# Kernel tuning notes

Measured on AMD Instinct MI355X. Metric: run time of the kernel, lower is better.

## Reference

```python
import jax, jax.numpy as jnp
import numpy as np

K = 3  # kernel_size
STRIDE, PAD, DIL = 1, 1, 1


def conv2d(x, w, b):
    out = jax.lax.conv_general_dilated(
        x, w, (STRIDE, STRIDE), [(PAD, PAD), (PAD, PAD)],
        rhs_dilation=(DIL, DIL), dimension_numbers=('NCHW', 'OIHW', 'NCHW'))
    return out + b[None, :, None, None]


def bilinear_sample(x, sy, sx):
    """grid_sample(mode=bilinear, padding_mode=zeros, align_corners=True).
    x: (B,C,H,W); sy,sx: (B,K2,Ho,Wo) pixel coords. Returns (B,C,K2,Ho,Wo)."""
    B, C, H, W = x.shape
    y0 = jnp.floor(sy); x0 = jnp.floor(sx)
    y1 = y0 + 1.0;      x1 = x0 + 1.0
    wy1 = sy - y0; wy0 = 1.0 - wy1
    wx1 = sx - x0; wx0 = 1.0 - wx1
    x_flat = x.reshape(B, C, H * W)

    def gather(iy, ix):
        mask = ((iy >= 0) & (iy <= H - 1) & (ix >= 0) & (ix <= W - 1)).astype(x.dtype)
        iyc = jnp.clip(iy, 0, H - 1).astype(jnp.int32)
        ixc = jnp.clip(ix, 0, W - 1).astype(jnp.int32)
        idx = (iyc * W + ixc).reshape(B, 1, -1)
        v = jnp.take_along_axis(x_flat, idx, axis=2).reshape(B, C, *iy.shape[1:])
        return v * mask[:, None]

    return (gather(y0, x0) * (wy0 * wx0)[:, None]
            + gather(y0, x1) * (wy0 * wx1)[:, None]
            + gather(y1, x0) * (wy1 * wx0)[:, None]
            + gather(y1, x1) * (wy1 * wx1)[:, None])


def setup_inputs() -> dict:
    key = jax.random.key(0)
    ks = jax.random.split(key, 6)
    B, C, H, W = 4, 64, 128, 128
    O = 64
    x = jax.random.normal(ks[0], (B, C, H, W), jnp.float32)
    weight = jax.random.normal(ks[1], (O, C, K, K), jnp.float32) * (1.0 / (C * K * K) ** 0.5)
    bias = jax.random.normal(ks[2], (O,), jnp.float32) * 0.1
    offset_w = jax.random.normal(ks[3], (2 * K * K, C, K, K), jnp.float32) * 0.1 / (C * K * K) ** 0.5
    offset_b = jnp.zeros((2 * K * K,), jnp.float32)
    mod_w = jax.random.normal(ks[4], (K * K, C, K, K), jnp.float32) * (1.0 / (C * K * K) ** 0.5)
    mod_b = jnp.ones((K * K,), jnp.float32)
    return {"x": x, "weight": weight, "bias": bias,
            "offset_w": offset_w, "offset_b": offset_b,
            "mod_w": mod_w, "mod_b": mod_b}


def reference(x, weight, bias, offset_w, offset_b, mod_w, mod_b):
    B, C, H, W = x.shape
    O = weight.shape[0]
    K2 = K * K
    Ho = (H + 2 * PAD - DIL * (K - 1) - 1) // STRIDE + 1
    Wo = (W + 2 * PAD - DIL * (K - 1) - 1) // STRIDE + 1

    offsets = conv2d(x, offset_w, offset_b)                # (B, 2*K2, Ho, Wo)
    modul = jax.nn.sigmoid(conv2d(x, mod_w, mod_b))        # (B, K2, Ho, Wo)

    off = offsets.reshape(B, 2, K2, Ho, Wo)
    off_y, off_x = off[:, 0], off[:, 1]

    base_y, base_x = jnp.meshgrid(jnp.arange(Ho, dtype=jnp.float32),
                                  jnp.arange(Wo, dtype=jnp.float32), indexing='ij')
    base_y = base_y * STRIDE - PAD + (K // 2) * DIL
    base_x = base_x * STRIDE - PAD + (K // 2) * DIL
    koffs = jnp.arange(-(K // 2), K // 2 + 1, dtype=jnp.float32)
    ky, kx = jnp.meshgrid(koffs, koffs, indexing='ij')
    ky = ky.reshape(-1); kx = kx.reshape(-1)               # (K2,)

    sample_y = base_y[None, None] + ky[None, :, None, None] + off_y  # (B,K2,Ho,Wo)
    sample_x = base_x[None, None] + kx[None, :, None, None] + off_x
    # torch code normalizes to [-1,1] with align_corners=True; pixel coords are
    # recovered identically, so we sample directly at (sample_y, sample_x).

    sampled = bilinear_sample(x, sample_y, sample_x)       # (B,C,K2,Ho,Wo)

    w_flat = weight.reshape(O, C, K2)
    out = jnp.einsum('bckhw,ock->bohw', sampled, w_flat)   # groups=1

    mod_mean = jnp.mean(modul, axis=1, keepdims=True)      # (B,1,Ho,Wo)
    out = out * mod_mean + bias[None, :, None, None]
    return out
```

## Files before the change

### kernel.cpp

```cpp
#include <hip/hip_runtime.h>
#include <math.h>

#define K 3
#define K2 9
#define BB 4
#define C 64
#define H 128
#define W 128
#define O 64
#define HW (H*W)
#define Ho 128
#define Wo 128
#define TILE 64
#define CG 16
#define NCHUNK 4
#define KCH 144
#define NSTEP 5
#define SA_STRIDE 164

typedef _Float16 half4v __attribute__((ext_vector_type(4)));
typedef _Float16 half8v __attribute__((ext_vector_type(8)));
typedef float float4v __attribute__((ext_vector_type(4)));

__device__ __forceinline__ half8v load_frag_lds(const _Float16* p) {
    half4v a = *(const half4v*)p;
    half4v b = *(const half4v*)(p + 4);
    return __builtin_shufflevector(a, b, 0, 1, 2, 3, 4, 5, 6, 7);
}
__device__ __forceinline__ void store16_lds(_Float16* d, half8v v) {
    *(half4v*)d       = __builtin_shufflevector(v, v, 0, 1, 2, 3);
    *(half4v*)(d + 4) = __builtin_shufflevector(v, v, 4, 5, 6, 7);
}

__global__ __launch_bounds__(256) void make_xh(const float* __restrict__ x,
                                               _Float16* __restrict__ xh)
{
    __shared__ _Float16 tile[W][68];
    int by = blockIdx.x;
    int y = by % H, b = by / H;
    int t = threadIdx.x;
    int xp = t & 127, ch0 = t >> 7;
    for (int g = 0; g < 32; g++) {
        int c = g * 2 + ch0;
        tile[xp][c] = (_Float16)x[(((size_t)b * C + c) * H + y) * W + xp];
    }
    __syncthreads();
    int xp2 = t >> 1, hf = t & 1;
    const _Float16* src = &tile[xp2][hf * 32];
    _Float16* dst = xh + (((size_t)b * H + y) * W + xp2) * 64 + hf * 32;
    #pragma unroll
    for (int i = 0; i < 8; i++)
        *(half4v*)(dst + i * 4) = *(const half4v*)(src + i * 4);
}

__global__ void prep_weights(const float* __restrict__ weight,
                             const float* __restrict__ offset_w,
                             const float* __restrict__ mod_w,
                             _Float16* __restrict__ wB,
                             _Float16* __restrict__ wAB)
{
    int i = blockIdx.x * blockDim.x + threadIdx.x;
    if (i < NCHUNK * NSTEP * 4 * 64 * 8) {
        int jj = i & 7;
        int lane = (i >> 3) & 63;
        int q = (i >> 9) & 3;
        int i2 = i >> 11;
        int cc = i2 / NSTEP, s = i2 % NSTEP;
        int k = s * 32 + ((lane >> 4) & 3) * 8 + jj;
        int o = q * 16 + (lane & 15);
        float wv = 0.f;
        if (k < KCH) {
            int tap = k >> 4, cl = k & 15;
            int c = cc * CG + cl;
            wv = weight[(o * C + c) * 9 + tap];
        }
        wB[i] = (_Float16)wv;
    }
    if (i < NCHUNK * NSTEP * 2 * 64 * 8) {
        int jj = i & 7;
        int lane = (i >> 3) & 63;
        int jt = (i >> 9) & 1;
        int i2 = i >> 10;
        int cc = i2 / NSTEP, s = i2 % NSTEP;
        int k = s * 32 + ((lane >> 4) & 3) * 8 + jj;
        int n = jt * 16 + (lane & 15);
        float wv = 0.f;
        if (k < KCH && n < 27) {
            int tap = k >> 4, cl = k & 15;
            int c = cc * CG + cl;
            wv = (n < 18) ? offset_w[(n * C + c) * 9 + tap]
                          : mod_w[((n - 18) * C + c) * 9 + tap];
        }
        wAB[i] = (_Float16)wv;
    }
}

__global__ __launch_bounds__(256) void fused_kernel(
    const _Float16* __restrict__ xh,
    const _Float16* __restrict__ wB,
    const _Float16* __restrict__ wAB,
    const float* __restrict__ bias,
    const float* __restrict__ offset_b,
    const float* __restrict__ mod_b,
    float* __restrict__ out)
{
    __shared__ _Float16 s_A[TILE][SA_STRIDE];
    __shared__ unsigned int s_ai[K2 * TILE];
    __shared__ float4v s_wgt[K2 * TILE];
    __shared__ float s_res[27 * 65];
    __shared__ float s_mm[TILE];
    float* s_out = (float*)&s_A[0][0];

    int blk = blockIdx.x;
    int xcd = blk & 7, idx = blk >> 3;
    int b  = xcd >> 1;
    int h  = ((xcd & 1) << 6) | (idx >> 1);
    int wt = idx & 1;
    int t  = threadIdx.x;
    int px = t & 63;
    int q  = t >> 6;
    int lane = t & 63;
    int m16 = lane & 15;
    int quad = (lane >> 4) & 3;
    int w0 = wt * TILE;
    int wp = w0 + px;

    for (int z = t; z < TILE * 16; z += 256)
        s_A[z >> 4][KCH + (z & 15)] = (_Float16)0.f;

    const _Float16* xb = xh + (size_t)b * HW * 64;

    float4v acc2[2];
    #pragma unroll
    for (int jt = 0; jt < 2; jt++) { float4v z = {0.f,0.f,0.f,0.f}; acc2[jt] = z; }

    #pragma unroll 1
    for (int cc = 0; cc < NCHUNK; cc++) {
        __syncthreads();
        #pragma unroll
        for (int ti = 0; ti < 3; ti++) {
            if (ti == 2 && q != 0) break;
            int tap = (ti < 2) ? (2 * q + ti) : 8;
            int ki = tap / 3, kj = tap % 3;
            int y = h + ki - 1;
            int xv = wp + kj - 1;
            float m = ((y >= 0 && y < H) ? 1.f : 0.f) * ((xv >= 0 && xv < W) ? 1.f : 0.f);
            int yc = min(max(y, 0), H - 1), xcl = min(max(xv, 0), W - 1);
            const _Float16* src = xb + ((size_t)yc * W + xcl) * 64 + cc * CG;
            half8v v0 = *(const half8v*)src;
            half8v v1 = *(const half8v*)(src + 8);
            _Float16 mh = (_Float16)m;
            half8v vm = {mh, mh, mh, mh, mh, mh, mh, mh};
            v0 *= vm; v1 *= vm;
            _Float16* d = &s_A[px][tap * 16];
            store16_lds(d, v0);
            store16_lds(d + 8, v1);
        }
        __syncthreads();

        int row = q * 16 + m16;
        #pragma unroll
        for (int s = 0; s < NSTEP; s++) {
            int koff = s * 32 + quad * 8;
            half8v af = load_frag_lds(&s_A[row][koff]);
            #pragma unroll
            for (int jt = 0; jt < 2; jt++) {
                int widx = (((cc * NSTEP + s) * 2 + jt) * 64 + lane) * 8;
                half8v bf = *(const half8v*)(wAB + widx);
                acc2[jt] = __builtin_amdgcn_mfma_f32_16x16x32_f16(af, bf, acc2[jt], 0, 0, 0);
            }
        }
    }
    __syncthreads();
    #pragma unroll
    for (int jt = 0; jt < 2; jt++) {
        int n = jt * 16 + m16;
        if (n < 27) {
            #pragma unroll
            for (int r = 0; r < 4; r++)
                s_res[n * 65 + q * 16 + quad * 4 + r] = acc2[jt][r];
        }
    }
    __syncthreads();

    #pragma unroll
    for (int ee = 0; ee < 3; ee++) {
        int e = t + ee * 256;
        if (e < K2 * TILE) {
            int k = e >> 6, p = e & 63;
            float offy = s_res[k * 65 + p] + offset_b[k];
            float offx = s_res[(9 + k) * 65 + p] + offset_b[9 + k];
            float sy = (float)(h + k / 3 - 1) + offy;
            float sx = (float)(w0 + p + k % 3 - 1) + offx;
            float fy = floorf(sy), fx = floorf(sx);
            int y0 = (int)fy, x0 = (int)fx;
            float wy1 = sy - fy, wx1 = sx - fx;
            int y0c = min(max(y0, 0), H - 1), y1c = min(max(y0 + 1, 0), H - 1);
            int x0c = min(max(x0, 0), W - 1), x1c = min(max(x0 + 1, 0), W - 1);
            s_ai[e] = (unsigned int)(y0c * W + x0c)
                    | ((unsigned int)(x1c - x0c) << 14)
                    | ((unsigned int)(y1c - y0c) << 15);
            float4v wg;
            wg[0] = (1.f - wy1) * ((y0 >= 0 && y0 < H) ? 1.f : 0.f);
            wg[1] = wy1 * ((y0 + 1 >= 0 && y0 + 1 < H) ? 1.f : 0.f);
            wg[2] = (1.f - wx1) * ((x0 >= 0 && x0 < W) ? 1.f : 0.f);
            wg[3] = wx1 * ((x0 + 1 >= 0 && x0 + 1 < W) ? 1.f : 0.f);
            s_wgt[e] = wg;
        }
    }
    if (t < TILE) {
        float sm = 0.f;
        #pragma unroll
        for (int m = 0; m < 9; m++) {
            float z = s_res[(18 + m) * 65 + t] + mod_b[m];
            sm += 1.f / (1.f + expf(-z));
        }
        s_mm[t] = sm * (1.f / 9.f);
    }

    float4v acc[4];
    #pragma unroll
    for (int i = 0; i < 4; i++) { float4v z = {0.f,0.f,0.f,0.f}; acc[i] = z; }

    #pragma unroll 1
    for (int cc = 0; cc < NCHUNK; cc++) {
        __syncthreads();
        #pragma unroll
        for (int ti = 0; ti < 3; ti++) {
            if (ti == 2 && q != 0) break;
            int tap = (ti < 2) ? (2 * q + ti) : 8;
            int e = tap * 64 + px;
            unsigned int ai = s_ai[e];
            float4v wg = s_wgt[e];
            float w00f = wg[0] * wg[2], w01f = wg[0] * wg[3];
            float w10f = wg[1] * wg[2], w11f = wg[1] * wg[3];
            int a00 = ai & 0x3FFF;
            int dxo = ((ai >> 14) & 1) * 64;
            int dyo = ((ai >> 15) & 1) * (W * 64);
            const _Float16* base = xb + (size_t)a00 * 64 + cc * CG;
            half8v r00a = *(const half8v*)(base);
            half8v r00b = *(const half8v*)(base + 8);
            half8v r01a = *(const half8v*)(base + dxo);
            half8v r01b = *(const half8v*)(base + dxo + 8);
            half8v r10a = *(const half8v*)(base + dyo);
            half8v r10b = *(const half8v*)(base + dyo + 8);
            half8v r11a = *(const half8v*)(base + dyo + dxo);
            half8v r11b = *(const half8v*)(base + dyo + dxo + 8);
            _Float16 w00 = (_Float16)w00f, w01 = (_Float16)w01f;
            _Float16 w10 = (_Float16)w10f, w11 = (_Float16)w11f;
            half8v vw00 = {w00,w00,w00,w00,w00,w00,w00,w00};
            half8v vw01 = {w01,w01,w01,w01,w01,w01,w01,w01};
            half8v vw10 = {w10,w10,w10,w10,w10,w10,w10,w10};
            half8v vw11 = {w11,w11,w11,w11,w11,w11,w11,w11};
            half8v va = r00a * vw00 + r01a * vw01 + r10a * vw10 + r11a * vw11;
            half8v vb = r00b * vw00 + r01b * vw01 + r10b * vw10 + r11b * vw11;
            _Float16* d = &s_A[px][tap * 16];
            store16_lds(d, va);
            store16_lds(d + 8, vb);
        }
        __syncthreads();

        #pragma unroll
        for (int s = 0; s < NSTEP; s++) {
            int widx = (((cc * NSTEP + s) * 4 + q) * 64 + lane) * 8;
            half8v bf = *(const half8v*)(wB + widx);
            int koff = s * 32 + quad * 8;
            #pragma unroll
            for (int i = 0; i < 4; i++) {
                half8v af = load_frag_lds(&s_A[i * 16 + m16][koff]);
                acc[i] = __builtin_amdgcn_mfma_f32_16x16x32_f16(af, bf, acc[i], 0, 0, 0);
            }
        }
    }

    __syncthreads();
    #pragma unroll
    for (int i = 0; i < 4; i++) {
        int o = q * 16 + m16;
        #pragma unroll
        for (int r = 0; r < 4; r++)
            s_out[o * 65 + i * 16 + quad * 4 + r] = acc[i][r];
    }
    __syncthreads();
    {
        float mm = s_mm[px];
        #pragma unroll
        for (int jj = 0; jj < 16; jj++) {
            int o = q * 16 + jj;
            out[(((size_t)b * O + o) * Ho + h) * Wo + w0 + px] =
                s_out[o * 65 + px] * mm + bias[o];
        }
    }
}

extern "C" void kernel_launch(void* const* d_in, const int* in_sizes, int n_in,
                              void* d_out, int out_size, void* d_ws, size_t ws_size,
                              hipStream_t stream) {
    const float* x        = (const float*)d_in[0];
    const float* weight   = (const float*)d_in[1];
    const float* bias     = (const float*)d_in[2];
    const float* offset_w = (const float*)d_in[3];
    const float* offset_b = (const float*)d_in[4];
    const float* mod_w    = (const float*)d_in[5];
    const float* mod_b    = (const float*)d_in[6];
    float* out = (float*)d_out;

    _Float16* wB  = (_Float16*)d_ws;
    _Float16* wAB = wB + 40960;
    _Float16* xh  = wAB + 20480;

    prep_weights<<<160, 256, 0, stream>>>(weight, offset_w, mod_w, wB, wAB);
    make_xh<<<BB * H, 256, 0, stream>>>(x, xh);

    int nblk = BB * Ho * (Wo / TILE);
    fused_kernel<<<nblk, 256, 0, stream>>>(
        xh, wB, wAB, bias, offset_b, mod_b, out);
}
```

Measured before the change: 134.8 us.

## Merge prep kernels, vectorize x loads, alias LDS, hoist per-tap address math

Combines the weight-repack and x-transpose kernels into one launch and switches the transpose to float4 global reads. In the fused kernel, s_res is aliased onto s_A to cut LDS use, and the bilinear weights are stored as precomputed fp16 products instead of fp32 factors. Per-tap source pointers, masks and gather offsets are now computed once outside the channel-chunk loops. The goals are less launch overhead, higher occupancy and less repeated integer work. The cost is more live registers and an extra barrier, plus re-zeroing the s_A pad columns because they now share memory with s_res.

Measured after the change: 148.2 us. 9.9% more time.

```diff
diff --git a/kernel.cpp b/kernel.cpp
--- a/kernel.cpp
+++ b/kernel.cpp
@@ -31,67 +31,77 @@
     *(half4v*)d       = __builtin_shufflevector(v, v, 0, 1, 2, 3);
     *(half4v*)(d + 4) = __builtin_shufflevector(v, v, 4, 5, 6, 7);
 }
-
-__global__ __launch_bounds__(256) void make_xh(const float* __restrict__ x,
-                                               _Float16* __restrict__ xh)
+__device__ __forceinline__ half8v bcast8(_Float16 w) {
+    half8v v = {w, w, w, w, w, w, w, w};
+    return v;
+}
+
+__global__ __launch_bounds__(256) void prep_all(
+    const float* __restrict__ x,
+    const float* __restrict__ weight,
+    const float* __restrict__ offset_w,
+    const float* __restrict__ mod_w,
+    _Float16* __restrict__ xh,
+    _Float16* __restrict__ wB,
+    _Float16* __restrict__ wAB)
 {
-    __shared__ _Float16 tile[W][68];
-    int by = blockIdx.x;
-    int y = by % H, b = by / H;
     int t = threadIdx.x;
-    int xp = t & 127, ch0 = t >> 7;
-    for (int g = 0; g < 32; g++) {
-        int c = g * 2 + ch0;
-        tile[xp][c] = (_Float16)x[(((size_t)b * C + c) * H + y) * W + xp];
-    }
-    __syncthreads();
-    int xp2 = t >> 1, hf = t & 1;
-    const _Float16* src = &tile[xp2][hf * 32];
-    _Float16* dst = xh + (((size_t)b * H + y) * W + xp2) * 64 + hf * 32;
-    #pragma unroll
-    for (int i = 0; i < 8; i++)
-        *(half4v*)(dst + i * 4) = *(const half4v*)(src + i * 4);
-}
-
-__global__ void prep_weights(const float* __restrict__ weight,
-                             const float* __restrict__ offset_w,
-                             const float* __restrict__ mod_w,
-                             _Float16* __restrict__ wB,
-                             _Float16* __restrict__ wAB)
-{
-    int i = blockIdx.x * blockDim.x + threadIdx.x;
-    if (i < NCHUNK * NSTEP * 4 * 64 * 8) {
-        int jj = i & 7;
-        int lane = (i >> 3) & 63;
-        int q = (i >> 9) & 3;
-        int i2 = i >> 11;
-        int cc = i2 / NSTEP, s = i2 % NSTEP;
-        int k = s * 32 + ((lane >> 4) & 3) * 8 + jj;
-        int o = q * 16 + (lane & 15);
-        float wv = 0.f;
-        if (k < KCH) {
-            int tap = k >> 4, cl = k & 15;
-            int c = cc * CG + cl;
-            wv = weight[(o * C + c) * 9 + tap];
-        }
-        wB[i] = (_Float16)wv;
-    }
-    if (i < NCHUNK * NSTEP * 2 * 64 * 8) {
-        int jj = i & 7;
-        int lane = (i >> 3) & 63;
-        int jt = (i >> 9) & 1;
-        int i2 = i >> 10;
-        int cc = i2 / NSTEP, s = i2 % NSTEP;
-        int k = s * 32 + ((lane >> 4) & 3) * 8 + jj;
-        int n = jt * 16 + (lane & 15);
-        float wv = 0.f;
-        if (k < KCH && n < 27) {
-            int tap = k >> 4, cl = k & 15;
-            int c = cc * CG + cl;
-            wv = (n < 18) ? offset_w[(n * C + c) * 9 + tap]
-                          : mod_w[((n - 18) * C + c) * 9 + tap];
-        }
-        wAB[i] = (_Float16)wv;
+    if (blockIdx.x < BB * H) {
+        __shared__ _Float16 tile[W][68];
+        int by = blockIdx.x;
+        int y = by % H, b = by / H;
+        int xq = t & 31, cr = t >> 5;
+        #pragma unroll
+        for (int g = 0; g < 8; g++) {
+            int c = g * 8 + cr;
+            float4v v = *(const float4v*)&x[(((size_t)b * C + c) * H + y) * W + xq * 4];
+            tile[xq * 4 + 0][c] = (_Float16)v[0];
+            tile[xq * 4 + 1][c] = (_Float16)v[1];
+            tile[xq * 4 + 2][c] = (_Float16)v[2];
+            tile[xq * 4 + 3][c] = (_Float16)v[3];
+        }
+        __syncthreads();
+        int xp2 = t >> 1, hf = t & 1;
+        const _Float16* src = &tile[xp2][hf * 32];
+        _Float16* dst = xh + (((size_t)b * H + y) * W + xp2) * 64 + hf * 32;
+        #pragma unroll
+        for (int i = 0; i < 8; i++)
+            *(half4v*)(dst + i * 4) = *(const half4v*)(src + i * 4);
+    } else {
+        int i = (blockIdx.x - BB * H) * 256 + t;
+        if (i < NCHUNK * NSTEP * 4 * 64 * 8) {
+            int jj = i & 7;
+            int lane = (i >> 3) & 63;
+            int q = (i >> 9) & 3;
+            int i2 = i >> 11;
+            int cc = i2 / NSTEP, s = i2 % NSTEP;
+            int k = s * 32 + ((lane >> 4) & 3) * 8 + jj;
+            int o = q * 16 + (lane & 15);
+            float wv = 0.f;
+            if (k < KCH) {
+                int tap = k >> 4, cl = k & 15;
+                int c = cc * CG + cl;
+                wv = weight[(o * C + c) * 9 + tap];
+            }
+            wB[i] = (_Float16)wv;
+        }
+        if (i < NCHUNK * NSTEP * 2 * 64 * 8) {
+            int jj = i & 7;
+            int lane = (i >> 3) & 63;
+            int jt = (i >> 9) & 1;
+            int i2 = i >> 10;
+            int cc = i2 / NSTEP, s = i2 % NSTEP;
+            int k = s * 32 + ((lane >> 4) & 3) * 8 + jj;
+            int n = jt * 16 + (lane & 15);
+            float wv = 0.f;
+            if (k < KCH && n < 27) {
+                int tap = k >> 4, cl = k & 15;
+                int c = cc * CG + cl;
+                wv = (n < 18) ? offset_w[(n * C + c) * 9 + tap]
+                              : mod_w[((n - 18) * C + c) * 9 + tap];
+            }
+            wAB[i] = (_Float16)wv;
+        }
     }
 }
 
@@ -106,9 +116,9 @@
 {
     __shared__ _Float16 s_A[TILE][SA_STRIDE];
     __shared__ unsigned int s_ai[K2 * TILE];
-    __shared__ float4v s_wgt[K2 * TILE];
-    __shared__ float s_res[27 * 65];
+    __shared__ half4v s_wgt[K2 * TILE];
     __shared__ float s_mm[TILE];
+    float* s_res = (float*)&s_A[0][0];
     float* s_out = (float*)&s_A[0][0];
 
     int blk = blockIdx.x;
@@ -130,6 +140,20 @@
 
     const _Float16* xb = xh + (size_t)b * HW * 64;
 
+    const _Float16* srcA[3];
+    _Float16 mhA[3];
+    #pragma unroll
+    for (int ti = 0; ti < 3; ti++) {
+        int tap = (ti < 2) ? (2 * q + ti) : 8;
+        int ki = tap / 3, kj = tap % 3;
+        int y = h + ki - 1;
+        int xv = wp + kj - 1;
+        float m = ((y >= 0 && y < H) ? 1.f : 0.f) * ((xv >= 0 && xv < W) ? 1.f : 0.f);
+        int yc = min(max(y, 0), H - 1), xcl = min(max(xv, 0), W - 1);
+        srcA[ti] = xb + ((size_t)yc * W + xcl) * 64;
+        mhA[ti] = (_Float16)m;
+    }
+
     float4v acc2[2];
     #pragma unroll
     for (int jt = 0; jt < 2; jt++) { float4v z = {0.f,0.f,0.f,0.f}; acc2[jt] = z; }
@@ -141,16 +165,10 @@
         for (int ti = 0; ti < 3; ti++) {
             if (ti == 2 && q != 0) break;
             int tap = (ti < 2) ? (2 * q + ti) : 8;
-            int ki = tap / 3, kj = tap % 3;
-            int y = h + ki - 1;
-            int xv = wp + kj - 1;
-            float m = ((y >= 0 && y < H) ? 1.f : 0.f) * ((xv >= 0 && xv < W) ? 1.f : 0.f);
-            int yc = min(max(y, 0), H - 1), xcl = min(max(xv, 0), W - 1);
-            const _Float16* src = xb + ((size_t)yc * W + xcl) * 64 + cc * CG;
+            const _Float16* src = srcA[ti] + cc * CG;
             half8v v0 = *(const half8v*)src;
             half8v v1 = *(const half8v*)(src + 8);
-            _Float16 mh = (_Float16)m;
-            half8v vm = {mh, mh, mh, mh, mh, mh, mh, mh};
+            half8v vm = bcast8(mhA[ti]);
             v0 *= vm; v1 *= vm;
             _Float16* d = &s_A[px][tap * 16];
             store16_lds(d, v0);
@@ -200,12 +218,16 @@
             s_ai[e] = (unsigned int)(y0c * W + x0c)
                     | ((unsigned int)(x1c - x0c) << 14)
                     | ((unsigned int)(y1c - y0c) << 15);
-            float4v wg;
-            wg[0] = (1.f - wy1) * ((y0 >= 0 && y0 < H) ? 1.f : 0.f);
-            wg[1] = wy1 * ((y0 + 1 >= 0 && y0 + 1 < H) ? 1.f : 0.f);
-            wg[2] = (1.f - wx1) * ((x0 >= 0 && x0 < W) ? 1.f : 0.f);
-            wg[3] = wx1 * ((x0 + 1 >= 0 && x0 + 1 < W) ? 1.f : 0.f);
-            s_wgt[e] = wg;
+            float wg0 = (1.f - wy1) * ((y0 >= 0 && y0 < H) ? 1.f : 0.f);
+            float wg1 = wy1 * ((y0 + 1 >= 0 && y0 + 1 < H) ? 1.f : 0.f);
+            float wg2 = (1.f - wx1) * ((x0 >= 0 && x0 < W) ? 1.f : 0.f);
+            float wg3 = wx1 * ((x0 + 1 >= 0 && x0 + 1 < W) ? 1.f : 0.f);
+            half4v wp4;
+            wp4[0] = (_Float16)(wg0 * wg2);
+            wp4[1] = (_Float16)(wg0 * wg3);
+            wp4[2] = (_Float16)(wg1 * wg2);
+            wp4[3] = (_Float16)(wg1 * wg3);
+            s_wgt[e] = wp4;
         }
     }
     if (t < TILE) {
@@ -217,6 +239,25 @@
         }
         s_mm[t] = sm * (1.f / 9.f);
     }
+    __syncthreads();
+
+    for (int z = t; z < TILE * 16; z += 256)
+        s_A[z >> 4][KCH + (z & 15)] = (_Float16)0.f;
+
+    const _Float16* baseC[3];
+    int dxoC[3], dyoC[3];
+    half4v wgC[3];
+    #pragma unroll
+    for (int ti = 0; ti < 3; ti++) {
+        int tap = (ti < 2) ? (2 * q + ti) : 8;
+        int e = tap * 64 + px;
+        unsigned int ai = s_ai[e];
+        wgC[ti] = s_wgt[e];
+        int a00 = ai & 0x3FFF;
+        dxoC[ti] = ((ai >> 14) & 1) * 64;
+        dyoC[ti] = ((ai >> 15) & 1) * (W * 64);
+        baseC[ti] = xb + (size_t)a00 * 64;
+    }
 
     float4v acc[4];
     #pragma unroll
@@ -229,15 +270,9 @@
         for (int ti = 0; ti < 3; ti++) {
             if (ti == 2 && q != 0) break;
             int tap = (ti < 2) ? (2 * q + ti) : 8;
-            int e = tap * 64 + px;
-            unsigned int ai = s_ai[e];
-            float4v wg = s_wgt[e];
-            float w00f = wg[0] * wg[2], w01f = wg[0] * wg[3];
-            float w10f = wg[1] * wg[2], w11f = wg[1] * wg[3];
-            int a00 = ai & 0x3FFF;
-            int dxo = ((ai >> 14) & 1) * 64;
-            int dyo = ((ai >> 15) & 1) * (W * 64);
-            const _Float16* base = xb + (size_t)a00 * 64 + cc * CG;
+            const _Float16* base = baseC[ti] + cc * CG;
+            int dxo = dxoC[ti], dyo = dyoC[ti];
+            half4v wg4 = wgC[ti];
             half8v r00a = *(const half8v*)(base);
             half8v r00b = *(const half8v*)(base + 8);
             half8v r01a = *(const half8v*)(base + dxo);
@@ -246,12 +281,8 @@
             half8v r10b = *(const half8v*)(base + dyo + 8);
             half8v r11a = *(const half8v*)(base + dyo + dxo);
             half8v r11b = *(const half8v*)(base + dyo + dxo + 8);
-            _Float16 w00 = (_Float16)w00f, w01 = (_Float16)w01f;
-            _Float16 w10 = (_Float16)w10f, w11 = (_Float16)w11f;
-            half8v vw00 = {w00,w00,w00,w00,w00,w00,w00,w00};
-            half8v vw01 = {w01,w01,w01,w01,w01,w01,w01,w01};
-            half8v vw10 = {w10,w10,w10,w10,w10,w10,w10,w10};
-            half8v vw11 = {w11,w11,w11,w11,w11,w11,w11,w11};
+            half8v vw00 = bcast8(wg4[0]), vw01 = bcast8(wg4[1]);
+            half8v vw10 = bcast8(wg4[2]), vw11 = bcast8(wg4[3]);
             half8v va = r00a * vw00 + r01a * vw01 + r10a * vw10 + r11a * vw11;
             half8v vb = r00b * vw00 + r01b * vw01 + r10b * vw10 + r11b * vw11;
             _Float16* d = &s_A[px][tap * 16];
@@ -309,8 +340,8 @@
     _Float16* wAB = wB + 40960;
     _Float16* xh  = wAB + 20480;
 
-    prep_weights<<<160, 256, 0, stream>>>(weight, offset_w, mod_w, wB, wAB);
-    make_xh<<<BB * H, 256, 0, stream>>>(x, xh);
+    prep_all<<<BB * H + 160, 256, 0, stream>>>(
+        x, weight, offset_w, mod_w, xh, wB, wAB);
 
     int nblk = BB * Ho * (Wo / TILE);
     fused_kernel<<<nblk, 256, 0, stream>>>(
```
